# Kernel optimization log

Hardware: AMD Instinct MI355X
Metric: run time of the kernel (lower is better)

The kernel has to match this reference:

```python
import jax, jax.numpy as jnp
import numpy as np

B, N1, N2 = 16, 4096, 1024
C1, C2 = 128, 256
IN_CH, OUT_CH = 4096, 256  # fc1 acts on N1 dim due to transpose; BN channels = C2 = OUT_CH
BN_EPS = 1e-5


def setup_inputs() -> dict:
    key = jax.random.key(0)
    ks = jax.random.split(key, 8)
    x1 = jax.random.normal(ks[0], (B, N1, C1), dtype=jnp.float32)
    x2 = jax.random.normal(ks[1], (B, N2, C2), dtype=jnp.float32)
    xyz1 = jax.random.normal(ks[2], (B, N1, 3), dtype=jnp.float32)
    xyz2 = jax.random.normal(ks[3], (B, N2, 3), dtype=jnp.float32)
    # Linear(in_channels=N1 -> out_channels) params, PyTorch default init scale
    bound = 1.0 / np.sqrt(IN_CH)
    W1 = jax.random.uniform(ks[4], (OUT_CH, IN_CH), jnp.float32, -bound, bound)
    b1 = jax.random.uniform(ks[5], (OUT_CH,), jnp.float32, -bound, bound)
    gamma = jnp.ones((OUT_CH,), jnp.float32)
    beta = jnp.zeros((OUT_CH,), jnp.float32)
    return {"x1": x1, "x2": x2, "xyz1": xyz1, "xyz2": xyz2,
            "W1": W1, "b1": b1, "gamma": gamma, "beta": beta}


def _square_distance(src, dst):
    # src: [B,N,3], dst: [B,M,3] -> [B,N,M]
    d = -2.0 * jnp.einsum('bnc,bmc->bnm', src, dst)
    d = d + jnp.sum(src * src, -1)[:, :, None]
    d = d + jnp.sum(dst * dst, -1)[:, None, :]
    return d


def reference(x1, x2, xyz1, xyz2, W1, b1, gamma, beta):
    dists = _square_distance(xyz1, xyz2)              # [B,N1,N2]
    neg3, idx = jax.lax.top_k(-dists, 3)              # 3 smallest distances
    d3 = -neg3                                        # [B,N1,3], ascending
    dist_recip = 1.0 / (d3 + 1e-8)
    weight = dist_recip / jnp.sum(dist_recip, axis=2, keepdims=True)
    gathered = jax.vmap(lambda pts, i: pts[i])(x2, idx)   # [B,N1,3,C2]
    interp = jnp.sum(gathered * weight[..., None], axis=2)  # [B,N1,C2]
    t = jnp.swapaxes(interp, 1, 2)                    # [B,C2,N1]
    y = jnp.einsum('bcn,on->bco', t, W1) + b1         # [B,C2,OUT_CH]
    # BatchNorm1d over channel dim 1 (size C2 == OUT_CH), training-mode batch stats
    mean = jnp.mean(y, axis=(0, 2), keepdims=True)
    var = jnp.mean((y - mean) ** 2, axis=(0, 2), keepdims=True)
    y = (y - mean) / jnp.sqrt(var + BN_EPS)
    y = gamma[None, :, None] * y + beta[None, :, None]
    y = jax.nn.relu(y)
    return jnp.swapaxes(y, 1, 2)                      # [B,OUT_CH,C2]
```

## Files before the change

### kernel.cpp

```cpp
#include <hip/hip_runtime.h>
#include <hip/hip_bf16.h>
#include <float.h>

#define B_    16
#define N1_   4096
#define N2_   1024
#define C2_   256
#define OUT_  256
#define K_    4096
#define SPLITK 8
#define KCH_  (K_ / SPLITK)
#define ZSLAB 1048576

typedef short short8 __attribute__((ext_vector_type(8)));
typedef float float4v __attribute__((ext_vector_type(4)));

static __device__ __forceinline__ unsigned short f32_to_bf16_bits(float v) {
    __hip_bfloat16 h = __float2bfloat16(v);
    return *(unsigned short*)&h;
}

__global__ __launch_bounds__(256) void w1cvt_kernel(
    const float* __restrict__ W1, unsigned short* __restrict__ W1b)
{
    const int i = (blockIdx.x * 256 + threadIdx.x) * 4;
    float4 v = *(const float4*)(W1 + i);
    ushort4 o;
    o.x = f32_to_bf16_bits(v.x);
    o.y = f32_to_bf16_bits(v.y);
    o.z = f32_to_bf16_bits(v.z);
    o.w = f32_to_bf16_bits(v.w);
    *(ushort4*)(W1b + i) = o;
}

#define TPAD 65
struct KnnSh {
    float4 pts[N2_];
    float  pf[4][64][3];
    int    pi[4][64][3];
};
union ShUnion {
    KnnSh a;
    unsigned short tile[C2_][TPAD];
};

__global__ __launch_bounds__(256) void knn_interp_kernel(
    const float* __restrict__ xyz1,
    const float* __restrict__ xyz2,
    const float* __restrict__ x2,
    unsigned short* __restrict__ interp_t)
{
    __shared__ ShUnion sh;
    __shared__ float rw[64][3];
    __shared__ int   ri[64][3];

    const int b  = blockIdx.y;
    const int n0 = blockIdx.x * 64;
    const int t  = threadIdx.x;
    const int w  = t >> 6;
    const int l  = t & 63;

    for (int r = 0; r < 4; ++r) {
        int j = r * 256 + t;
        const float* p = xyz2 + ((size_t)b * N2_ + j) * 3;
        float x = p[0], y = p[1], z = p[2];
        sh.a.pts[j] = make_float4(x, y, z, 0.5f * ((x * x + y * y) + z * z));
    }
    __syncthreads();

    const int n1 = n0 + l;
    const float* q = xyz1 + ((size_t)b * N1_ + n1) * 3;
    const float s0 = q[0], s1 = q[1], s2 = q[2];

    float f0 = FLT_MAX, f1 = FLT_MAX, f2 = FLT_MAX;
    int   i0 = 0, i1 = 0, i2 = 0;
    const int jbase = w * 256;

    #pragma unroll 4
    for (int jj = 0; jj < 256; ++jj) {
        const int j = jbase + jj;
        float4 pq = sh.a.pts[j];
        float dot = s0 * pq.x;
        dot = fmaf(s1, pq.y, dot);
        dot = fmaf(s2, pq.z, dot);
        float f = pq.w - dot;
        bool c0 = f < f0, c1 = f < f1, c2 = f < f2;
        f2 = c1 ? f1 : (c2 ? f : f2);  i2 = c1 ? i1 : (c2 ? j : i2);
        f1 = c0 ? f0 : (c1 ? f : f1);  i1 = c0 ? i0 : (c1 ? j : i1);
        f0 = c0 ? f  : f0;             i0 = c0 ? j  : i0;
    }

    sh.a.pf[w][l][0] = f0; sh.a.pf[w][l][1] = f1; sh.a.pf[w][l][2] = f2;
    sh.a.pi[w][l][0] = i0; sh.a.pi[w][l][1] = i1; sh.a.pi[w][l][2] = i2;
    __syncthreads();

    if (w == 0) {
        float g0 = FLT_MAX, g1 = FLT_MAX, g2 = FLT_MAX;
        int   j0 = 0, j1 = 0, j2 = 0;
        #pragma unroll
        for (int p = 0; p < 4; ++p)
        #pragma unroll
        for (int r = 0; r < 3; ++r) {
            float f = sh.a.pf[p][l][r];
            int   j = sh.a.pi[p][l][r];
            bool c0 = f < g0, c1 = f < g1, c2 = f < g2;
            g2 = c1 ? g1 : (c2 ? f : g2);  j2 = c1 ? j1 : (c2 ? j : j2);
            g1 = c0 ? g0 : (c1 ? f : g1);  j1 = c0 ? j0 : (c1 ? j : j1);
            g0 = c0 ? f  : g0;             j0 = c0 ? j  : j0;
        }
        const float ss = (s0 * s0 + s1 * s1) + s2 * s2;
        float d0 = ss + 2.0f * g0;
        float d1 = ss + 2.0f * g1;
        float d2 = ss + 2.0f * g2;
        float r0 = 1.0f / (d0 + 1e-8f);
        float r1 = 1.0f / (d1 + 1e-8f);
        float r2 = 1.0f / (d2 + 1e-8f);
        float s  = (r0 + r1) + r2;
        rw[l][0] = r0 / s;  rw[l][1] = r1 / s;  rw[l][2] = r2 / s;
        ri[l][0] = j0;      ri[l][1] = j1;      ri[l][2] = j2;
    }
    __syncthreads();

    for (int p = 0; p < 16; ++p) {
        int nl = p * 4 + w;
        float w0 = rw[nl][0], w1 = rw[nl][1], w2 = rw[nl][2];
        int i0g = ri[nl][0], i1g = ri[nl][1], i2g = ri[nl][2];
        const float4 va = ((const float4*)(x2 + ((size_t)b * N2_ + i0g) * C2_))[l];
        const float4 vb = ((const float4*)(x2 + ((size_t)b * N2_ + i1g) * C2_))[l];
        const float4 vc = ((const float4*)(x2 + ((size_t)b * N2_ + i2g) * C2_))[l];
        float fa[4] = {va.x, va.y, va.z, va.w};
        float fb[4] = {vb.x, vb.y, vb.z, vb.w};
        float fc[4] = {vc.x, vc.y, vc.z, vc.w};
        #pragma unroll
        for (int i = 0; i < 4; ++i) {
            float v = w0 * fa[i];
            v = fmaf(w1, fb[i], v);
            v = fmaf(w2, fc[i], v);
            sh.tile[l * 4 + i][nl] = f32_to_bf16_bits(v);
        }
    }
    __syncthreads();

    for (int r = 0; r < 64; ++r) {
        int c = r * 4 + w;
        interp_t[((size_t)b * C2_ + c) * K_ + n0 + l] = sh.tile[c][l];
    }
}

#define LDA 40
__global__ __launch_bounds__(256) void gemm_kernel(
    const unsigned short* __restrict__ W1b,
    const unsigned short* __restrict__ interp_t,
    float* __restrict__ Zp)
{
    __shared__ unsigned short Alds[64][LDA];
    __shared__ unsigned short Blds[64][LDA];
    const int z  = blockIdx.z;
    const int b  = z >> 3;
    const int kc = z & 7;
    const int o0 = blockIdx.y * 64;
    const int c0 = blockIdx.x * 64;
    const int t = threadIdx.x;
    const int w = t >> 6, l = t & 63;
    const int row = t >> 2, q = t & 3;
    const int ob = (w >> 1) * 32, cb = (w & 1) * 32;
    const int m = l & 15, kq = l >> 4;

    const unsigned short* Wp = W1b + (size_t)(o0 + row) * K_ + kc * KCH_ + q * 8;
    const unsigned short* Bp = interp_t + ((size_t)b * C2_ + (c0 + row)) * K_ + kc * KCH_ + q * 8;

    float4v acc[2][2] = {};

    for (int kk = 0; kk < KCH_; kk += 32) {
        uint4 av = *(const uint4*)(Wp + kk);
        uint4 bv = *(const uint4*)(Bp + kk);
        *(uint4*)&Alds[row][q * 8] = av;
        *(uint4*)&Blds[row][q * 8] = bv;
        __syncthreads();
        short8 a0 = *(const short8*)&Alds[ob + m][kq * 8];
        short8 a1 = *(const short8*)&Alds[ob + 16 + m][kq * 8];
        short8 b0 = *(const short8*)&Blds[cb + m][kq * 8];
        short8 b1f = *(const short8*)&Blds[cb + 16 + m][kq * 8];
        acc[0][0] = __builtin_amdgcn_mfma_f32_16x16x32_bf16(a0, b0,  acc[0][0], 0, 0, 0);
        acc[0][1] = __builtin_amdgcn_mfma_f32_16x16x32_bf16(a0, b1f, acc[0][1], 0, 0, 0);
        acc[1][0] = __builtin_amdgcn_mfma_f32_16x16x32_bf16(a1, b0,  acc[1][0], 0, 0, 0);
        acc[1][1] = __builtin_amdgcn_mfma_f32_16x16x32_bf16(a1, b1f, acc[1][1], 0, 0, 0);
        __syncthreads();
    }

    float* Zslab = Zp + (size_t)kc * ZSLAB;
    #pragma unroll
    for (int mi = 0; mi < 2; ++mi)
    #pragma unroll
    for (int ni = 0; ni < 2; ++ni)
    #pragma unroll
    for (int r = 0; r < 4; ++r) {
        int o = o0 + ob + mi * 16 + kq * 4 + r;
        int c = c0 + cb + ni * 16 + m;
        Zslab[((size_t)b * OUT_ + o) * C2_ + c] = acc[mi][ni][r];
    }
}

__global__ __launch_bounds__(256) void reduce_stats_kernel(
    float* __restrict__ Zp, const float* __restrict__ b1,
    float* __restrict__ accum)
{
    const int b  = blockIdx.x >> 4;
    const int oq = blockIdx.x & 15;
    const int c  = threadIdx.x;
    float s = 0.0f, s2 = 0.0f;
    for (int o16 = 0; o16 < 16; ++o16) {
        int o = oq * 16 + o16;
        size_t base = ((size_t)b * OUT_ + o) * C2_ + c;
        float v = b1[o];
        #pragma unroll
        for (int sl = 0; sl < SPLITK; ++sl)
            v += Zp[base + (size_t)sl * ZSLAB];
        Zp[base] = v;
        s += v; s2 += v * v;
    }
    atomicAdd(&accum[c], s);
    atomicAdd(&accum[C2_ + c], s2);
}

__global__ __launch_bounds__(256) void bn_kernel(
    const float* __restrict__ Z, const float* __restrict__ accum,
    const float* __restrict__ gamma, const float* __restrict__ beta,
    float* __restrict__ out)
{
    const int i = (blockIdx.x * 256 + threadIdx.x) * 4;
    float4 z = *(const float4*)(Z + i);
    float vals[4] = {z.x, z.y, z.z, z.w};
    const int cb = i & 255;
    float res[4];
    #pragma unroll
    for (int j = 0; j < 4; ++j) {
        int c = cb + j;
        float mean = accum[c] * (1.0f / 4096.0f);
        float var  = accum[C2_ + c] * (1.0f / 4096.0f) - mean * mean;
        float rstd = 1.0f / sqrtf(var + 1e-5f);
        float v = gamma[c] * ((vals[j] - mean) * rstd) + beta[c];
        res[j] = fmaxf(v, 0.0f);
    }
    *(float4*)(out + i) = make_float4(res[0], res[1], res[2], res[3]);
}

extern "C" void kernel_launch(void* const* d_in, const int* in_sizes, int n_in,
                              void* d_out, int out_size, void* d_ws, size_t ws_size,
                              hipStream_t stream) {
    const float* x2    = (const float*)d_in[1];
    const float* xyz1  = (const float*)d_in[2];
    const float* xyz2  = (const float*)d_in[3];
    const float* W1    = (const float*)d_in[4];
    const float* b1    = (const float*)d_in[5];
    const float* gamma = (const float*)d_in[6];
    const float* beta  = (const float*)d_in[7];

    char* ws = (char*)d_ws;
    unsigned short* interp_t = (unsigned short*)(ws);
    unsigned short* W1b      = (unsigned short*)(ws + 33554432);
    float*          Zp       = (float*)(ws + 35651584);
    float*          accum    = (float*)(ws + 69206016);

    (void)hipMemsetAsync(accum, 0, 512 * sizeof(float), stream);

    w1cvt_kernel      <<<1024, 256, 0, stream>>>(W1, W1b);
    knn_interp_kernel <<<dim3(64, 16), 256, 0, stream>>>(xyz1, xyz2, x2, interp_t);
    gemm_kernel       <<<dim3(4, 4, 128), 256, 0, stream>>>(W1b, interp_t, Zp);
    reduce_stats_kernel<<<256, 256, 0, stream>>>(Zp, b1, accum);
    bn_kernel         <<<1024, 256, 0, stream>>>(Zp, accum, gamma, beta,
                                                 (float*)d_out);
}
```

Baseline: 172.9 us.

## Pack neighbor index into distance bits and use min/med3 top-3 selection

The kNN inner loop now computes the full squared distance, clamps it at zero, and overwrites its low 10 mantissa bits with the candidate index. This lets a branchless fminf/fmed3/fmax network maintain the top-3 without separate index registers or selects. Point preprocessing (the float4 with the half-norm) moves into its own small kernel, and the kNN loop reads those points from global memory with a wave-uniform base instead of staging them in LDS. The exact distances for the three winners are recomputed afterwards. Truncating mantissa bits can change neighbor order when distances are nearly tied, and the loop now depends on global/cache loads instead of LDS.

```diff
diff --git a/kernel.cpp b/kernel.cpp
--- a/kernel.cpp
+++ b/kernel.cpp
@@ -33,20 +33,24 @@
     *(ushort4*)(W1b + i) = o;
 }
 
+__global__ __launch_bounds__(256) void ptsprep_kernel(
+    const float* __restrict__ xyz2, float4* __restrict__ pts4)
+{
+    const int i = blockIdx.x * 256 + threadIdx.x;
+    const float* p = xyz2 + (size_t)i * 3;
+    float x = p[0], y = p[1], z = p[2];
+    pts4[i] = make_float4(x, y, z, 0.5f * ((x * x + y * y) + z * z));
+}
+
 #define TPAD 65
-struct KnnSh {
-    float4 pts[N2_];
-    float  pf[4][64][3];
-    int    pi[4][64][3];
-};
 union ShUnion {
-    KnnSh a;
+    float pf[4][64][3];
     unsigned short tile[C2_][TPAD];
 };
 
 __global__ __launch_bounds__(256) void knn_interp_kernel(
     const float* __restrict__ xyz1,
-    const float* __restrict__ xyz2,
+    const float4* __restrict__ pts4,
     const float* __restrict__ x2,
     unsigned short* __restrict__ interp_t)
 {
@@ -60,58 +64,54 @@
     const int w  = t >> 6;
     const int l  = t & 63;
 
-    for (int r = 0; r < 4; ++r) {
-        int j = r * 256 + t;
-        const float* p = xyz2 + ((size_t)b * N2_ + j) * 3;
-        float x = p[0], y = p[1], z = p[2];
-        sh.a.pts[j] = make_float4(x, y, z, 0.5f * ((x * x + y * y) + z * z));
-    }
-    __syncthreads();
-
     const int n1 = n0 + l;
     const float* q = xyz1 + ((size_t)b * N1_ + n1) * 3;
     const float s0 = q[0], s1 = q[1], s2 = q[2];
+    const float ss = (s0 * s0 + s1 * s1) + s2 * s2;
+
+    const int jbase = __builtin_amdgcn_readfirstlane(w << 8);
+    const float4* pw = pts4 + (size_t)b * N2_ + jbase;
 
     float f0 = FLT_MAX, f1 = FLT_MAX, f2 = FLT_MAX;
-    int   i0 = 0, i1 = 0, i2 = 0;
-    const int jbase = w * 256;
 
     #pragma unroll 4
     for (int jj = 0; jj < 256; ++jj) {
-        const int j = jbase + jj;
-        float4 pq = sh.a.pts[j];
+        float4 pq = pw[jj];
         float dot = s0 * pq.x;
         dot = fmaf(s1, pq.y, dot);
         dot = fmaf(s2, pq.z, dot);
-        float f = pq.w - dot;
-        bool c0 = f < f0, c1 = f < f1, c2 = f < f2;
-        f2 = c1 ? f1 : (c2 ? f : f2);  i2 = c1 ? i1 : (c2 ? j : i2);
-        f1 = c0 ? f0 : (c1 ? f : f1);  i1 = c0 ? i0 : (c1 ? j : i1);
-        f0 = c0 ? f  : f0;             i0 = c0 ? j  : i0;
-    }
-
-    sh.a.pf[w][l][0] = f0; sh.a.pf[w][l][1] = f1; sh.a.pf[w][l][2] = f2;
-    sh.a.pi[w][l][0] = i0; sh.a.pi[w][l][1] = i1; sh.a.pi[w][l][2] = i2;
+        float dk = fmaxf(fmaf(2.0f, pq.w - dot, ss), 0.0f);
+        float fp = __int_as_float((__float_as_int(dk) & 0xFFFFFC00) | (jbase + jj));
+        float nf0 = fminf(fp, f0);
+        float nf1 = __builtin_amdgcn_fmed3f(fp, f0, f1);
+        float nf2 = fminf(f2, fmaxf(fp, f1));
+        f0 = nf0; f1 = nf1; f2 = nf2;
+    }
+
+    sh.pf[w][l][0] = f0; sh.pf[w][l][1] = f1; sh.pf[w][l][2] = f2;
     __syncthreads();
 
     if (w == 0) {
         float g0 = FLT_MAX, g1 = FLT_MAX, g2 = FLT_MAX;
-        int   j0 = 0, j1 = 0, j2 = 0;
         #pragma unroll
         for (int p = 0; p < 4; ++p)
         #pragma unroll
         for (int r = 0; r < 3; ++r) {
-            float f = sh.a.pf[p][l][r];
-            int   j = sh.a.pi[p][l][r];
-            bool c0 = f < g0, c1 = f < g1, c2 = f < g2;
-            g2 = c1 ? g1 : (c2 ? f : g2);  j2 = c1 ? j1 : (c2 ? j : j2);
-            g1 = c0 ? g0 : (c1 ? f : g1);  j1 = c0 ? j0 : (c1 ? j : j1);
-            g0 = c0 ? f  : g0;             j0 = c0 ? j  : j0;
+            float fp = sh.pf[p][l][r];
+            float n0v = fminf(fp, g0);
+            float n1v = __builtin_amdgcn_fmed3f(fp, g0, g1);
+            float n2v = fminf(g2, fmaxf(fp, g1));
+            g0 = n0v; g1 = n1v; g2 = n2v;
         }
-        const float ss = (s0 * s0 + s1 * s1) + s2 * s2;
-        float d0 = ss + 2.0f * g0;
-        float d1 = ss + 2.0f * g1;
-        float d2 = ss + 2.0f * g2;
+        int j0 = __float_as_int(g0) & 1023;
+        int j1 = __float_as_int(g1) & 1023;
+        int j2 = __float_as_int(g2) & 1023;
+        const float4 p0 = pts4[(size_t)b * N2_ + j0];
+        const float4 p1 = pts4[(size_t)b * N2_ + j1];
+        const float4 p2 = pts4[(size_t)b * N2_ + j2];
+        float d0 = ss + 2.0f * (p0.w - ((s0 * p0.x + s1 * p0.y) + s2 * p0.z));
+        float d1 = ss + 2.0f * (p1.w - ((s0 * p1.x + s1 * p1.y) + s2 * p1.z));
+        float d2 = ss + 2.0f * (p2.w - ((s0 * p2.x + s1 * p2.y) + s2 * p2.z));
         float r0 = 1.0f / (d0 + 1e-8f);
         float r1 = 1.0f / (d1 + 1e-8f);
         float r2 = 1.0f / (d2 + 1e-8f);
@@ -260,12 +260,14 @@
     unsigned short* interp_t = (unsigned short*)(ws);
     unsigned short* W1b      = (unsigned short*)(ws + 33554432);
     float*          Zp       = (float*)(ws + 35651584);
-    float*          accum    = (float*)(ws + 69206016);
+    float4*         pts4     = (float4*)(ws + 69206016);
+    float*          accum    = (float*)(ws + 69468160);
 
     (void)hipMemsetAsync(accum, 0, 512 * sizeof(float), stream);
 
     w1cvt_kernel      <<<1024, 256, 0, stream>>>(W1, W1b);
-    knn_interp_kernel <<<dim3(64, 16), 256, 0, stream>>>(xyz1, xyz2, x2, interp_t);
+    ptsprep_kernel    <<<64, 256, 0, stream>>>(xyz2, pts4);
+    knn_interp_kernel <<<dim3(64, 16), 256, 0, stream>>>(xyz1, pts4, x2, interp_t);
     gemm_kernel       <<<dim3(4, 4, 128), 256, 0, stream>>>(W1b, interp_t, Zp);
     reduce_stats_kernel<<<256, 256, 0, stream>>>(Zp, b1, accum);
     bn_kernel         <<<1024, 256, 0, stream>>>(Zp, accum, gamma, beta,
```

After: 184.6 us. 1.07x slower.
